# Kernel tuning notes

Measured on AMD Instinct MI355X. Metric: run time of the kernel, lower is better.

The kernel has to match this reference:

```python
import jax, jax.numpy as jnp
import numpy as np


def conv2d(x, w, b, pad):
    y = jax.lax.conv_general_dilated(x, w, (1, 1), [(pad, pad), (pad, pad)],
                                     dimension_numbers=('NCHW', 'OIHW', 'NCHW'))
    return y + b[None, :, None, None]


def setup_inputs() -> dict:
    key = jax.random.key(0)
    ks = jax.random.split(key, 24)
    bs, C, OC, K = 2, 64, 3, 3
    hi = wi = 96
    ho = wo = 192

    def _w(k, o, i, kh, kw):
        return jax.random.normal(k, (o, i, kh, kw), jnp.float32) / np.float32(np.sqrt(i * kh * kw))

    inp = {
        'x': jax.random.normal(ks[0], (bs, C, hi, wi), jnp.float32),
        'poseMap': jax.random.normal(ks[1], (1, 3, ho, wo), jnp.float32),
        'interMapY': jax.random.randint(ks[2], (ho, wo), 0, hi, jnp.int32),
        'interMapX': jax.random.randint(ks[3], (ho, wo), 0, wi, jnp.int32),
        # sigmaconv: 3x3 convs 64->64->64->2
        'sig_w1': _w(ks[4], 64, 64, 3, 3), 'sig_b1': jnp.zeros((64,), jnp.float32),
        'sig_w2': _w(ks[5], 64, 64, 3, 3), 'sig_b2': jnp.zeros((64,), jnp.float32),
        'sig_w3': _w(ks[6], 2, 64, 3, 3), 'sig_b3': jnp.zeros((2,), jnp.float32),
        # dwconv: 1x1 convs 3->64->256->C*K*K
        'dw_w1': _w(ks[7], 64, 3, 1, 1), 'dw_b1': jnp.zeros((64,), jnp.float32),
        'dw_w2': _w(ks[8], 256, 64, 1, 1), 'dw_b2': jnp.zeros((256,), jnp.float32),
        'dw_w3': _w(ks[9], C * K * K, 256, 1, 1), 'dw_b3': jnp.zeros((C * K * K,), jnp.float32),
        # pwconv: 1x1 convs 3->64->256->C*OC
        'pw_w1': _w(ks[10], 64, 3, 1, 1), 'pw_b1': jnp.zeros((64,), jnp.float32),
        'pw_w2': _w(ks[11], 256, 64, 1, 1), 'pw_b2': jnp.zeros((256,), jnp.float32),
        'pw_w3': _w(ks[12], C * OC, 256, 1, 1), 'pw_b3': jnp.zeros((C * OC,), jnp.float32),
    }
    return inp


def reference(x, poseMap, interMapY, interMapX,
              sig_w1, sig_b1, sig_w2, sig_b2, sig_w3, sig_b3,
              dw_w1, dw_b1, dw_w2, dw_b2, dw_w3, dw_b3,
              pw_w1, pw_b1, pw_w2, pw_b2, pw_w3, pw_b3):
    C, K, OC = 64, 3, 3
    bs, _, hi, wi = x.shape
    ho, wo = poseMap.shape[2], poseMap.shape[3]
    pad = K // 2

    p = jax.lax.stop_gradient(poseMap)  # original detaches poseMap
    # kernel-predict branches (1x1 conv MLPs over position map)
    dw = conv2d(jax.nn.relu(conv2d(jax.nn.relu(conv2d(p, dw_w1, dw_b1, 0)), dw_w2, dw_b2, 0)), dw_w3, dw_b3, 0)
    dw = dw.reshape(1, C, K * K, ho, wo)
    pw = conv2d(jax.nn.relu(conv2d(jax.nn.relu(conv2d(p, pw_w1, pw_b1, 0)), pw_w2, pw_b2, 0)), pw_w3, pw_b3, 0)
    pw = pw.reshape(C, OC, ho, wo)

    # unfold(x, K, padding=K//2): [bs, C, K*K, hi, wi], kernel taps row-major
    xp = jnp.pad(x, ((0, 0), (0, 0), (pad, pad), (pad, pad)))
    h = jnp.stack([xp[:, :, dy:dy + hi, dx:dx + wi]
                   for dy in range(K) for dx in range(K)], axis=2)
    # irregular spatial gather to HR grid: [bs, C, K*K, ho, wo]
    h = h[:, :, :, interMapY, interMapX]

    mean = jnp.sum(h * jax.nn.softmax(dw, axis=2), axis=2)  # [bs, C, ho, wo]
    sigma = conv2d(jax.nn.relu(conv2d(jax.nn.relu(conv2d(mean, sig_w1, sig_b1, 1)), sig_w2, sig_b2, 1)), sig_w3, sig_b3, 1)
    sigmad = sigma[:, 0:1, None, :, :]
    sigmar = sigma[:, 1:2, None, :, :]
    bw = sigmad * dw + sigmar * jnp.abs(h - mean[:, :, None, :, :])
    xa = jnp.sum(h * jax.nn.softmax(bw, axis=2), axis=2)  # [bs, C, ho, wo]
    out = jnp.einsum('bchw,cohw->bohw', xa, pw)  # [bs, OC, ho, wo]
    return out
```

## Files before the change

### kernel.cpp

```cpp
#include <hip/hip_runtime.h>
#include <hip/hip_bf16.h>

#define NPIX 36864

typedef __attribute__((ext_vector_type(8))) short short8;
typedef __attribute__((ext_vector_type(4))) short short4v;
typedef __attribute__((ext_vector_type(4))) float float4v;

__device__ inline unsigned short f2b(float x) {
    return __builtin_bit_cast(unsigned short, __float2bfloat16(x));
}
__device__ inline float b2f(unsigned short h) {
    return __uint_as_float(((unsigned int)h) << 16);
}

#define WB_TOTAL 312320
#define XCAST_N  1179648
__global__ __launch_bounds__(256) void prep_all(
    const float* __restrict__ dw2, const float* __restrict__ dw3,
    const float* __restrict__ pw2, const float* __restrict__ pw3,
    const float* __restrict__ sw1, const float* __restrict__ sw2,
    const float* __restrict__ sw3, unsigned short* __restrict__ wb,
    const float* __restrict__ x, unsigned short* __restrict__ xb)
{
    int i = blockIdx.x * 256 + threadIdx.x;
    if (i >= WB_TOTAL) {
        int j = i - WB_TOTAL;
        if (j < XCAST_N) xb[j] = f2b(x[j]);
        return;
    }
    unsigned short v;
    if (i < 16384)        v = f2b(dw2[i]);
    else if (i < 32768)   v = f2b(pw2[i - 16384]);
    else if (i < 180224)  v = f2b(dw3[i - 32768]);
    else if (i < 229376)  v = f2b(pw3[i - 180224]);
    else if (i < 266240) { int j = i - 229376; int t = j / 4096, r = j % 4096, oc = r / 64, ic = r % 64;
                           v = f2b(sw1[(oc * 64 + ic) * 9 + t]); }
    else if (i < 303104) { int j = i - 266240; int t = j / 4096, r = j % 4096, oc = r / 64, ic = r % 64;
                           v = f2b(sw2[(oc * 64 + ic) * 9 + t]); }
    else                 { int j = i - 303104; int t = j / 1024, r = j % 1024, oc = r / 64, ic = r % 64;
                           v = (oc < 2) ? f2b(sw3[(oc * 64 + ic) * 9 + t]) : (unsigned short)0; }
    wb[i] = v;
}

__global__ __launch_bounds__(512, 2) void mlp_fused(
    const float* __restrict__ pose,
    const float* __restrict__ w1A, const float* __restrict__ b1A,
    const float* __restrict__ w1B, const float* __restrict__ b1B,
    const unsigned short* __restrict__ w2A, const unsigned short* __restrict__ w2B,
    const float* __restrict__ b2A, const float* __restrict__ b2B,
    const unsigned short* __restrict__ w33,
    const float* __restrict__ b3A, const float* __restrict__ b3B,
    unsigned short* __restrict__ outA, unsigned short* __restrict__ outB)
{
    __shared__ unsigned short sh[69632];
    unsigned short* Ws  = sh;
    unsigned short* h2s = sh + 49152;
    unsigned short* h1s = sh + 65536;
    const int tid = threadIdx.x;
    const int u = blockIdx.y;
    const int chain = (u == 3) ? 1 : 0;
    const int w = tid >> 6, l = tid & 63;
    const int ln = l & 15, lkg = l >> 4, lk = lkg * 8;
    const float* w1 = chain ? w1B : w1A;
    const float* b1 = chain ? b1B : b1A;
    const unsigned short* w2 = chain ? w2B : w2A;
    const float* b2 = chain ? b2B : b2A;
    const int rowbase = chain ? 576 : u * 192;
    const int obase   = chain ? 0 : u * 192;
    const float* b3 = chain ? b3B : b3A;
    unsigned short* outp = chain ? outB : outA;

    for (int i = 0; i < 12; ++i) {
        const int chunk = (i * 8 + w) * 1024;
        int a  = chunk + l * 16;
        int ap = a ^ (((a >> 9) & 7) << 4);
        const unsigned short* gp =
            &w33[(size_t)(rowbase + (ap >> 9)) * 256 + ((ap & 511) >> 1)];
        __builtin_amdgcn_global_load_lds(
            (const __attribute__((address_space(1))) void*)gp,
            (__attribute__((address_space(3))) void*)((char*)Ws + chunk),
            16, 0, 0);
    }
    short8 Aw2[2][2];
    #pragma unroll
    for (int mt = 0; mt < 2; ++mt) {
        int ocr = w * 32 + mt * 16 + ln;
        Aw2[mt][0] = *(const short8*)&w2[(size_t)ocr * 64 + lk];
        Aw2[mt][1] = *(const short8*)&w2[(size_t)ocr * 64 + 32 + lk];
    }
    float w1r[8][3], b1r[8];
    #pragma unroll
    for (int j = 0; j < 8; ++j) {
        int oc = w * 8 + j;
        w1r[j][0] = w1[oc * 3]; w1r[j][1] = w1[oc * 3 + 1]; w1r[j][2] = w1[oc * 3 + 2];
        b1r[j] = b1[oc];
    }
    float b2r[2][4];
    #pragma unroll
    for (int mt = 0; mt < 2; ++mt) {
        int ocb = w * 32 + mt * 16 + lkg * 4;
        #pragma unroll
        for (int r = 0; r < 4; ++r) b2r[mt][r] = b2[ocb + r];
    }
    const int nh = w & 1, mb = w >> 1;
    float b3r[3][4];
    #pragma unroll
    for (int s = 0; s < 3; ++s) {
        int tr0 = (mb + s * 4) * 16 + lkg * 4;
        #pragma unroll
        for (int r = 0; r < 4; ++r) b3r[s][r] = b3[obase + tr0 + r];
    }
    const int pxbase = blockIdx.x * 576;
    float p0 = pose[pxbase + l], p1 = pose[NPIX + pxbase + l], p2 = pose[2 * NPIX + pxbase + l];

    for (int it = 0; it < 9; ++it) {
        const int px0 = pxbase + it * 64;
        {
            short8 s0;
            #pragma unroll
            for (int j = 0; j < 8; ++j) {
                float v = b1r[j] + w1r[j][0] * p0 + w1r[j][1] * p1 + w1r[j][2] * p2;
                s0[j] = (short)f2b(fmaxf(v, 0.f));
            }
            *(short8*)&h1s[w * 512 + l * 8] = s0;
        }
        float np0 = 0.f, np1 = 0.f, np2 = 0.f;
        if (it < 8) {
            int pxn = px0 + 64 + l;
            np0 = pose[pxn]; np1 = pose[NPIX + pxn]; np2 = pose[2 * NPIX + pxn];
        }
        __syncthreads();
        {
            short8 b0v[4], b1v[4];
            #pragma unroll
            for (int nt = 0; nt < 4; ++nt) {
                b0v[nt] = *(const short8*)&h1s[(lkg    ) * 512 + (nt * 16 + ln) * 8];
                b1v[nt] = *(const short8*)&h1s[(4 + lkg) * 512 + (nt * 16 + ln) * 8];
            }
            float4v acc2[2][4] = {};
            #pragma unroll
            for (int mt = 0; mt < 2; ++mt) {
                #pragma unroll
                for (int nt = 0; nt < 4; ++nt) {
                    acc2[mt][nt] = __builtin_amdgcn_mfma_f32_16x16x32_bf16(Aw2[mt][0], b0v[nt], acc2[mt][nt], 0, 0, 0);
                    acc2[mt][nt] = __builtin_amdgcn_mfma_f32_16x16x32_bf16(Aw2[mt][1], b1v[nt], acc2[mt][nt], 0, 0, 0);
                }
            }
            #pragma unroll
            for (int mt = 0; mt < 2; ++mt) {
                int ocb = w * 32 + mt * 16 + lkg * 4;
                int chk = ocb >> 3, pos = (lkg & 1) * 4;
                #pragma unroll
                for (int nt = 0; nt < 4; ++nt) {
                    int pxl = nt * 16 + ln;
                    short4v pk;
                    pk[0] = (short)f2b(fmaxf(acc2[mt][nt][0] + b2r[mt][0], 0.f));
                    pk[1] = (short)f2b(fmaxf(acc2[mt][nt][1] + b2r[mt][1], 0.f));
                    pk[2] = (short)f2b(fmaxf(acc2[mt][nt][2] + b2r[mt][2], 0.f));
                    pk[3] = (short)f2b(fmaxf(acc2[mt][nt][3] + b2r[mt][3], 0.f));
                    *(short4v*)&h2s[chk * 512 + pxl * 8 + pos] = pk;
                }
            }
        }
        __syncthreads();
        float4v acc[3][2] = {};
        {
            const int r0l = mb * 16 + ln;
            const int swz = (r0l & 7) << 4;
            const char* Wb = (const char*)Ws;
            #pragma unroll
            for (int kc = 0; kc < 8; ++kc) {
                short8 a0 = *(const short8*)(Wb + (((r0l      ) * 512 + kc * 64 + lk * 2) ^ swz));
                short8 a1 = *(const short8*)(Wb + (((r0l +  64) * 512 + kc * 64 + lk * 2) ^ swz));
                short8 a2 = *(const short8*)(Wb + (((r0l + 128) * 512 + kc * 64 + lk * 2) ^ swz));
                #pragma unroll
                for (int ni = 0; ni < 2; ++ni) {
                    int nt = nh * 2 + ni;
                    short8 b = *(const short8*)&h2s[(kc * 4 + lkg) * 512 + (nt * 16 + ln) * 8];
                    acc[0][ni] = __builtin_amdgcn_mfma_f32_16x16x32_bf16(a0, b, acc[0][ni], 0, 0, 0);
                    acc[1][ni] = __builtin_amdgcn_mfma_f32_16x16x32_bf16(a1, b, acc[1][ni], 0, 0, 0);
                    acc[2][ni] = __builtin_amdgcn_mfma_f32_16x16x32_bf16(a2, b, acc[2][ni], 0, 0, 0);
                }
            }
        }
        #pragma unroll
        for (int s = 0; s < 3; ++s) {
            const int tr0 = (mb + s * 4) * 16 + lkg * 4;
            #pragma unroll
            for (int r = 0; r < 4; ++r) {
                const size_t rowoff = (size_t)(obase + tr0 + r) * NPIX + px0;
                #pragma unroll
                for (int ni = 0; ni < 2; ++ni) {
                    int px = nh * 32 + ni * 16 + ln;
                    outp[rowoff + px] = f2b(acc[s][ni][r] + b3r[s][r]);
                }
            }
        }
        p0 = np0; p1 = np1; p2 = np2;
    }
}

__global__ __launch_bounds__(256, 2) void conv3x3_mfma4(
    const unsigned short* __restrict__ act, const unsigned short* __restrict__ wgt,
    const float* __restrict__ bias, unsigned short* __restrict__ out,
    int relu)
{
    constexpr int SP = 72;
    __shared__ unsigned short Bs[6 * 66 * SP];
    const int tid = threadIdx.x;
    int bx = blockIdx.x;
    const int xt = bx % 3; bx /= 3;
    const int yg = bx % 48; const int b = bx / 48;
    const int y0 = yg * 4;
    const int x0 = xt * 64;
    const size_t actb = (size_t)b * NPIX * 64;
    const int w = tid >> 6, l = tid & 63;
    const int ln = l & 15, lkg = l >> 4, lk = lkg * 8;
    const int mt = w;
    short8 Wr[9][2];
    #pragma unroll
    for (int t = 0; t < 9; ++t)
        #pragma unroll
        for (int hh = 0; hh < 2; ++hh)
            Wr[t][hh] = *(const short8*)&wgt[((size_t)t * 64 + mt * 16 + ln) * 64 + hh * 32 + lk];
    for (int s = tid; s < 396; s += 256) {
        int r = s / 66, i = s % 66;
        int yy = y0 + r - 1, xx = x0 + i - 1;
        unsigned short* dst = &Bs[(r * 66 + i) * SP];
        if (yy >= 0 && yy < 192 && xx >= 0 && xx < 192) {
            const unsigned short* src = &act[actb + (size_t)(yy * 192 + xx) * 64];
            #pragma unroll
            for (int j = 0; j < 8; ++j) *(short8*)(dst + j * 8) = *(const short8*)(src + j * 8);
        } else {
            short8 z = {};
            #pragma unroll
            for (int j = 0; j < 8; ++j) *(short8*)(dst + j * 8) = z;
        }
    }
    __syncthreads();
    float4v acc[4][4] = {};
    #pragma unroll
    for (int rp = 0; rp < 6; ++rp) {
        #pragma unroll
        for (int dx = 0; dx < 3; ++dx) {
            #pragma unroll
            for (int hh = 0; hh < 2; ++hh) {
                #pragma unroll
                for (int n = 0; n < 4; ++n) {
                    int slot = rp * 66 + n * 16 + ln + dx;
                    short8 bf = *(const short8*)&Bs[slot * SP + hh * 32 + lk];
                    #pragma unroll
                    for (int o = 0; o < 4; ++o) {
                        int r = rp - o;
                        if (r < 0 || r > 2) continue;
                        acc[o][n] = __builtin_amdgcn_mfma_f32_16x16x32_bf16(Wr[r * 3 + dx][hh], bf, acc[o][n], 0, 0, 0);
                    }
                }
            }
        }
    }
    #pragma unroll
    for (int o = 0; o < 4; ++o) {
        #pragma unroll
        for (int n = 0; n < 4; ++n) {
            int px = (y0 + o) * 192 + x0 + n * 16 + ln;
            int oc = mt * 16 + lkg * 4;
            float v0 = acc[o][n][0] + bias[oc + 0];
            float v1 = acc[o][n][1] + bias[oc + 1];
            float v2 = acc[o][n][2] + bias[oc + 2];
            float v3 = acc[o][n][3] + bias[oc + 3];
            if (relu) { v0 = fmaxf(v0, 0.f); v1 = fmaxf(v1, 0.f); v2 = fmaxf(v2, 0.f); v3 = fmaxf(v3, 0.f); }
            uint2 pk;
            pk.x = (unsigned int)f2b(v0) | (((unsigned int)f2b(v1)) << 16);
            pk.y = (unsigned int)f2b(v2) | (((unsigned int)f2b(v3)) << 16);
            *(uint2*)&out[((size_t)b * NPIX + px) * 64 + oc] = pk;
        }
    }
}

template<int MT>
__global__ __launch_bounds__(256) void conv3x3_mfma(
    const unsigned short* __restrict__ act, const unsigned short* __restrict__ wgt,
    const float* __restrict__ bias, unsigned short* __restrict__ out,
    int relu)
{
    constexpr int SP = 72;
    constexpr int OCP = MT * 16;
    __shared__ unsigned short Bs[4 * 66 * SP];
    const int tid = threadIdx.x;
    int bx = blockIdx.x;
    const int xt = bx % 3; bx /= 3;
    const int yg = bx % 96; const int b = bx / 96;
    const int y0 = yg * 2;
    const int x0 = xt * 64;
    const size_t actb = (size_t)b * NPIX * 64;
    const int w = tid >> 6, l = tid & 63;
    const int ln = l & 15, lkg = l >> 4, lk = lkg * 8;
    const int mt = (MT == 4) ? w : 0;
    short8 Wr[9][2];
    #pragma unroll
    for (int t = 0; t < 9; ++t)
        #pragma unroll
        for (int hh = 0; hh < 2; ++hh)
            Wr[t][hh] = *(const short8*)&wgt[((size_t)t * OCP + mt * 16 + ln) * 64 + hh * 32 + lk];
    for (int s = tid; s < 264; s += 256) {
        int r = s / 66, i = s % 66;
        int yy = y0 + r - 1, xx = x0 + i - 1;
        unsigned short* dst = &Bs[(r * 66 + i) * SP];
        if (yy >= 0 && yy < 192 && xx >= 0 && xx < 192) {
            const unsigned short* src = &act[actb + (size_t)(yy * 192 + xx) * 64];
            #pragma unroll
            for (int j = 0; j < 8; ++j) *(short8*)(dst + j * 8) = *(const short8*)(src + j * 8);
        } else {
            short8 z = {};
            #pragma unroll
            for (int j = 0; j < 8; ++j) *(short8*)(dst + j * 8) = z;
        }
    }
    __syncthreads();
    const int NT = (MT == 4) ? 4 : 1;
    const int ntb = (MT == 4) ? 0 : w;
    float4v acc[2][4] = {};
    #pragma unroll
    for (int t = 0; t < 9; ++t) {
        const int r = t / 3, dx = t % 3;
        #pragma unroll
        for (int hh = 0; hh < 2; ++hh) {
            #pragma unroll
            for (int o = 0; o < 2; ++o) {
                #pragma unroll
                for (int n = 0; n < 4; ++n) {
                    if (n >= NT) break;
                    int slot = (o + r) * 66 + (ntb + n) * 16 + ln + dx;
                    short8 bf = *(const short8*)&Bs[slot * SP + hh * 32 + lk];
                    acc[o][n] = __builtin_amdgcn_mfma_f32_16x16x32_bf16(Wr[t][hh], bf, acc[o][n], 0, 0, 0);
                }
            }
        }
    }
    #pragma unroll
    for (int o = 0; o < 2; ++o) {
        #pragma unroll
        for (int n = 0; n < 4; ++n) {
            if (n >= NT) break;
            int px = (y0 + o) * 192 + x0 + (ntb + n) * 16 + ln;
            if (MT == 4) {
                int oc = mt * 16 + lkg * 4;
                float v0 = acc[o][n][0] + bias[oc + 0];
                float v1 = acc[o][n][1] + bias[oc + 1];
                float v2 = acc[o][n][2] + bias[oc + 2];
                float v3 = acc[o][n][3] + bias[oc + 3];
                if (relu) { v0 = fmaxf(v0, 0.f); v1 = fmaxf(v1, 0.f); v2 = fmaxf(v2, 0.f); v3 = fmaxf(v3, 0.f); }
                uint2 pk;
                pk.x = (unsigned int)f2b(v0) | (((unsigned int)f2b(v1)) << 16);
                pk.y = (unsigned int)f2b(v2) | (((unsigned int)f2b(v3)) << 16);
                *(uint2*)&out[((size_t)b * NPIX + px) * 64 + oc] = pk;
            } else if (lkg == 0) {
                float v0 = acc[o][n][0] + bias[0];
                float v1 = acc[o][n][1] + bias[1];
                out[((size_t)b * 2 + 0) * NPIX + px] = f2b(v0);
                out[((size_t)b * 2 + 1) * NPIX + px] = f2b(v1);
            }
        }
    }
}

#define PLSZ 10192
__global__ __launch_bounds__(256) void mean_k(
    const unsigned short* __restrict__ xb, const int* __restrict__ imy, const int* __restrict__ imx,
    const unsigned short* __restrict__ dw, unsigned short* __restrict__ mean_cm)
{
    __shared__ unsigned short pl[PLSZ];
    const int c = blockIdx.y;
    const int px0 = blockIdx.x * 1024;
    const int tid = threadIdx.x;
    {
        short8 z = {};
        short8* pf = (short8*)pl;
        for (int i = tid; i < PLSZ / 8; i += 256) pf[i] = z;
    }
    float wk[4][9];
    int base[4];
    #pragma unroll
    for (int q = 0; q < 4; ++q) {
        int px = px0 + q * 256 + tid;
        base[q] = imy[px] * 104 + imx[px] + 3;
        float d[9];
        #pragma unroll
        for (int k = 0; k < 9; ++k) d[k] = b2f(dw[(size_t)(c * 9 + k) * NPIX + px]);
        float m = d[0];
        #pragma unroll
        for (int k = 1; k < 9; ++k) m = fmaxf(m, d[k]);
        float s = 0.f;
        #pragma unroll
        for (int k = 0; k < 9; ++k) { wk[q][k] = __expf(d[k] - m); s += wk[q][k]; }
        float inv = 1.f / s;
        #pragma unroll
        for (int k = 0; k < 9; ++k) wk[q][k] *= inv;
    }
    #pragma unroll
    for (int b = 0; b < 2; ++b) {
        __syncthreads();
        const unsigned short* xp = xb + (size_t)(b * 64 + c) * 9216;
        for (int i = tid; i < 96 * 12; i += 256) {
            int row = i / 12, ch = i % 12;
            const short4v* src = (const short4v*)&xp[row * 96 + ch * 8];
            unsigned short* dd = &pl[(row + 1) * 104 + 4 + ch * 8];
            *(short4v*)dd = src[0];
            *(short4v*)(dd + 4) = src[1];
        }
        __syncthreads();
        #pragma unroll
        for (int q = 0; q < 4; ++q) {
            int px = px0 + q * 256 + tid;
            float a = 0.f;
            #pragma unroll
            for (int k = 0; k < 9; ++k)
                a += wk[q][k] * b2f(pl[base[q] + (k / 3) * 104 + (k % 3)]);
            mean_cm[(size_t)(b * 64 + c) * NPIX + px] = f2b(a);
        }
    }
}

__global__ __launch_bounds__(256) void tr_k(
    const unsigned short* __restrict__ in, unsigned short* __restrict__ out)
{
    __shared__ unsigned short T[64 * 68];
    int px0 = blockIdx.x * 64;
    int b = blockIdx.y;
    int tid = threadIdx.x;
    for (int i = tid; i < 4096; i += 256) {
        int c = i >> 6, p = i & 63;
        T[p * 68 + c] = in[(size_t)(b * 64 + c) * NPIX + px0 + p];
    }
    __syncthreads();
    for (int i = tid; i < 4096; i += 256) {
        int p = i >> 6, c = i & 63;
        out[((size_t)b * NPIX + px0 + p) * 64 + c] = T[p * 68 + c];
    }
}

__global__ __launch_bounds__(256) void xa_k(
    const unsigned short* __restrict__ xb, const int* __restrict__ imy, const int* __restrict__ imx,
    const unsigned short* __restrict__ dw, const unsigned short* __restrict__ mean_cm,
    const unsigned short* __restrict__ sigma, unsigned short* __restrict__ xab)
{
    __shared__ unsigned short pl[PLSZ];
    const int c = blockIdx.y;
    const int px0 = blockIdx.x * 1024;
    const int tid = threadIdx.x;
    {
        short8 z = {};
        short8* pf = (short8*)pl;
        for (int i = tid; i < PLSZ / 8; i += 256) pf[i] = z;
    }
    float d[4][9];
    int base[4];
    #pragma unroll
    for (int q = 0; q < 4; ++q) {
        int px = px0 + q * 256 + tid;
        base[q] = imy[px] * 104 + imx[px] + 3;
        #pragma unroll
        for (int k = 0; k < 9; ++k) d[q][k] = b2f(dw[(size_t)(c * 9 + k) * NPIX + px]);
    }
    #pragma unroll
    for (int b = 0; b < 2; ++b) {
        __syncthreads();
        const unsigned short* xp = xb + (size_t)(b * 64 + c) * 9216;
        for (int i = tid; i < 96 * 12; i += 256) {
            int row = i / 12, ch = i % 12;
            const short4v* src = (const short4v*)&xp[row * 96 + ch * 8];
            unsigned short* dd = &pl[(row + 1) * 104 + 4 + ch * 8];
            *(short4v*)dd = src[0];
            *(short4v*)(dd + 4) = src[1];
        }
        __syncthreads();
        #pragma unroll
        for (int q = 0; q < 4; ++q) {
            int px = px0 + q * 256 + tid;
            float mn = b2f(mean_cm[(size_t)(b * 64 + c) * NPIX + px]);
            float sd = b2f(sigma[((size_t)b * 2 + 0) * NPIX + px]);
            float sr = b2f(sigma[((size_t)b * 2 + 1) * NPIX + px]);
            float h[9], bw[9];
            #pragma unroll
            for (int k = 0; k < 9; ++k) {
                h[k] = b2f(pl[base[q] + (k / 3) * 104 + (k % 3)]);
                bw[k] = sd * d[q][k] + sr * fabsf(h[k] - mn);
            }
            float m = bw[0];
            #pragma unroll
            for (int k = 1; k < 9; ++k) m = fmaxf(m, bw[k]);
            float s = 0.f, a = 0.f;
            #pragma unroll
            for (int k = 0; k < 9; ++k) { float e = __expf(bw[k] - m); s += e; a += e * h[k]; }
            xab[(size_t)(b * 64 + c) * NPIX + px] = f2b(a / s);
        }
    }
}

__global__ __launch_bounds__(256) void einsum_k(
    const unsigned short* __restrict__ xab, const unsigned short* __restrict__ pw,
    float* __restrict__ out)
{
    __shared__ float red[3][4][64];
    const int tid = threadIdx.x;
    const int pxl = tid & 63, cq = tid >> 6;
    const int px = blockIdx.x * 64 + pxl;
    const int b = blockIdx.y;
    float a0 = 0.f, a1 = 0.f, a2 = 0.f;
    #pragma unroll
    for (int ci = 0; ci < 16; ++ci) {
        int c = cq * 16 + ci;
        float v = b2f(xab[(size_t)(b * 64 + c) * NPIX + px]);
        a0 += v * b2f(pw[(size_t)(c * 3 + 0) * NPIX + px]);
        a1 += v * b2f(pw[(size_t)(c * 3 + 1) * NPIX + px]);
        a2 += v * b2f(pw[(size_t)(c * 3 + 2) * NPIX + px]);
    }
    red[0][cq][pxl] = a0;
    red[1][cq][pxl] = a1;
    red[2][cq][pxl] = a2;
    __syncthreads();
    if (cq < 3) {
        float s = red[cq][0][pxl] + red[cq][1][pxl] + red[cq][2][pxl] + red[cq][3][pxl];
        out[((size_t)b * 3 + cq) * NPIX + px] = s;
    }
}

extern "C" void kernel_launch(void* const* d_in, const int* in_sizes, int n_in,
                              void* d_out, int out_size, void* d_ws, size_t ws_size,
                              hipStream_t stream)
{
    (void)in_sizes; (void)n_in; (void)out_size; (void)ws_size;
    const float* x      = (const float*)d_in[0];
    const float* pose   = (const float*)d_in[1];
    const int*   imy    = (const int*)d_in[2];
    const int*   imx    = (const int*)d_in[3];
    const float* sig_w1 = (const float*)d_in[4];
    const float* sig_b1 = (const float*)d_in[5];
    const float* sig_w2 = (const float*)d_in[6];
    const float* sig_b2 = (const float*)d_in[7];
    const float* sig_w3 = (const float*)d_in[8];
    const float* sig_b3 = (const float*)d_in[9];
    const float* dw_w1  = (const float*)d_in[10];
    const float* dw_b1  = (const float*)d_in[11];
    const float* dw_w2  = (const float*)d_in[12];
    const float* dw_b2  = (const float*)d_in[13];
    const float* dw_w3  = (const float*)d_in[14];
    const float* dw_b3  = (const float*)d_in[15];
    const float* pw_w1  = (const float*)d_in[16];
    const float* pw_b1  = (const float*)d_in[17];
    const float* pw_w2  = (const float*)d_in[18];
    const float* pw_b2  = (const float*)d_in[19];
    const float* pw_w3  = (const float*)d_in[20];
    const float* pw_b3  = (const float*)d_in[21];
    float* out = (float*)d_out;

    unsigned short* ws = (unsigned short*)d_ws;
    size_t off = 0;
    unsigned short* wb      = ws + off; off += WB_TOTAL;
    unsigned short* xb16    = ws + off; off += (size_t)XCAST_N;
    unsigned short* dwbuf   = ws + off; off += (size_t)576 * NPIX;
    unsigned short* pwbuf   = ws + off; off += (size_t)192 * NPIX;
    unsigned short* mean_cm = ws + off; off += (size_t)2 * 64 * NPIX;
    unsigned short* mean_pm = ws + off; off += (size_t)2 * NPIX * 64;
    unsigned short* s1      = ws + off; off += (size_t)2 * NPIX * 64;
    unsigned short* s2      = ws + off; off += (size_t)2 * NPIX * 64;
    unsigned short* sigma   = ws + off; off += (size_t)2 * 2 * NPIX;
    unsigned short* xab     = ws + off; off += (size_t)2 * 64 * NPIX;

    unsigned short* w_dw2 = wb + 0;
    unsigned short* w_pw2 = wb + 16384;
    unsigned short* w_33  = wb + 32768;
    unsigned short* w_s1t = wb + 229376;
    unsigned short* w_s2t = wb + 266240;
    unsigned short* w_s3t = wb + 303104;

    dim3 blk(256);
    prep_all<<<dim3((WB_TOTAL + XCAST_N + 255) / 256), blk, 0, stream>>>(
        dw_w2, dw_w3, pw_w2, pw_w3, sig_w1, sig_w2, sig_w3, wb, x, xb16);
    mlp_fused<<<dim3(64, 4), dim3(512), 0, stream>>>(
        pose, dw_w1, dw_b1, pw_w1, pw_b1, w_dw2, w_pw2, dw_b2, pw_b2,
        w_33, dw_b3, pw_b3, dwbuf, pwbuf);
    mean_k<<<dim3(36, 64), blk, 0, stream>>>(xb16, imy, imx, dwbuf, mean_cm);
    tr_k<<<dim3(576, 2), blk, 0, stream>>>(mean_cm, mean_pm);
    conv3x3_mfma4<<<dim3(288), blk, 0, stream>>>(mean_pm, w_s1t, sig_b1, s1, 1);
    conv3x3_mfma4<<<dim3(288), blk, 0, stream>>>(s1,      w_s2t, sig_b2, s2, 1);
    conv3x3_mfma<1><<<dim3(576), blk, 0, stream>>>(s2,     w_s3t, sig_b3, sigma, 0);
    xa_k<<<dim3(36, 64), blk, 0, stream>>>(xb16, imy, imx, dwbuf, mean_cm, sigma, xab);
    einsum_k<<<dim3(576, 2), blk, 0, stream>>>(xab, pwbuf, out);
}
```

Before: 228.6 us.

## Remove prep kernel by converting weights and input to bf16 inside consumers

The separate prep_all launch that cast weights and x to bf16 into workspace is removed. Each consumer kernel (mlp_fused, conv3x3, mean_k, xa_k) now reads the fp32 tensors directly and converts them in registers before staging to LDS or loading MFMA operands. This saves one launch and a round-trip write and read of the bf16 copies. In exchange, fp32 reads double the bytes per element, conversion work is repeated across blocks, the conv weight loads become strided scalar gathers, and the async global_load_lds path for w3 is replaced by synchronous loads.

```diff
diff --git a/kernel.cpp b/kernel.cpp
--- a/kernel.cpp
+++ b/kernel.cpp
@@ -12,44 +12,15 @@
 }
 __device__ inline float b2f(unsigned short h) {
     return __uint_as_float(((unsigned int)h) << 16);
-}
-
-#define WB_TOTAL 312320
-#define XCAST_N  1179648
-__global__ __launch_bounds__(256) void prep_all(
-    const float* __restrict__ dw2, const float* __restrict__ dw3,
-    const float* __restrict__ pw2, const float* __restrict__ pw3,
-    const float* __restrict__ sw1, const float* __restrict__ sw2,
-    const float* __restrict__ sw3, unsigned short* __restrict__ wb,
-    const float* __restrict__ x, unsigned short* __restrict__ xb)
-{
-    int i = blockIdx.x * 256 + threadIdx.x;
-    if (i >= WB_TOTAL) {
-        int j = i - WB_TOTAL;
-        if (j < XCAST_N) xb[j] = f2b(x[j]);
-        return;
-    }
-    unsigned short v;
-    if (i < 16384)        v = f2b(dw2[i]);
-    else if (i < 32768)   v = f2b(pw2[i - 16384]);
-    else if (i < 180224)  v = f2b(dw3[i - 32768]);
-    else if (i < 229376)  v = f2b(pw3[i - 180224]);
-    else if (i < 266240) { int j = i - 229376; int t = j / 4096, r = j % 4096, oc = r / 64, ic = r % 64;
-                           v = f2b(sw1[(oc * 64 + ic) * 9 + t]); }
-    else if (i < 303104) { int j = i - 266240; int t = j / 4096, r = j % 4096, oc = r / 64, ic = r % 64;
-                           v = f2b(sw2[(oc * 64 + ic) * 9 + t]); }
-    else                 { int j = i - 303104; int t = j / 1024, r = j % 1024, oc = r / 64, ic = r % 64;
-                           v = (oc < 2) ? f2b(sw3[(oc * 64 + ic) * 9 + t]) : (unsigned short)0; }
-    wb[i] = v;
 }
 
 __global__ __launch_bounds__(512, 2) void mlp_fused(
     const float* __restrict__ pose,
     const float* __restrict__ w1A, const float* __restrict__ b1A,
     const float* __restrict__ w1B, const float* __restrict__ b1B,
-    const unsigned short* __restrict__ w2A, const unsigned short* __restrict__ w2B,
+    const float* __restrict__ w2Af, const float* __restrict__ w2Bf,
     const float* __restrict__ b2A, const float* __restrict__ b2B,
-    const unsigned short* __restrict__ w33,
+    const float* __restrict__ w3Af, const float* __restrict__ w3Bf,
     const float* __restrict__ b3A, const float* __restrict__ b3B,
     unsigned short* __restrict__ outA, unsigned short* __restrict__ outB)
 {
@@ -64,10 +35,11 @@
     const int ln = l & 15, lkg = l >> 4, lk = lkg * 8;
     const float* w1 = chain ? w1B : w1A;
     const float* b1 = chain ? b1B : b1A;
-    const unsigned short* w2 = chain ? w2B : w2A;
+    const float* w2f = chain ? w2Bf : w2Af;
     const float* b2 = chain ? b2B : b2A;
-    const int rowbase = chain ? 576 : u * 192;
-    const int obase   = chain ? 0 : u * 192;
+    const float* w3f = chain ? w3Bf : w3Af;
+    const int rb    = chain ? 0 : u * 192;
+    const int obase = chain ? 0 : u * 192;
     const float* b3 = chain ? b3B : b3A;
     unsigned short* outp = chain ? outB : outA;
 
@@ -75,19 +47,32 @@
         const int chunk = (i * 8 + w) * 1024;
         int a  = chunk + l * 16;
         int ap = a ^ (((a >> 9) & 7) << 4);
-        const unsigned short* gp =
-            &w33[(size_t)(rowbase + (ap >> 9)) * 256 + ((ap & 511) >> 1)];
-        __builtin_amdgcn_global_load_lds(
-            (const __attribute__((address_space(1))) void*)gp,
-            (__attribute__((address_space(3))) void*)((char*)Ws + chunk),
-            16, 0, 0);
+        const float* gp = &w3f[(size_t)(rb + (ap >> 9)) * 256 + ((ap & 511) >> 1)];
+        float4v f0 = *(const float4v*)gp;
+        float4v f1 = *(const float4v*)(gp + 4);
+        short8 s;
+        s[0] = (short)f2b(f0[0]); s[1] = (short)f2b(f0[1]);
+        s[2] = (short)f2b(f0[2]); s[3] = (short)f2b(f0[3]);
+        s[4] = (short)f2b(f1[0]); s[5] = (short)f2b(f1[1]);
+        s[6] = (short)f2b(f1[2]); s[7] = (short)f2b(f1[3]);
+        *(short8*)((char*)Ws + a) = s;
     }
     short8 Aw2[2][2];
     #pragma unroll
     for (int mt = 0; mt < 2; ++mt) {
         int ocr = w * 32 + mt * 16 + ln;
-        Aw2[mt][0] = *(const short8*)&w2[(size_t)ocr * 64 + lk];
-        Aw2[mt][1] = *(const short8*)&w2[(size_t)ocr * 64 + 32 + lk];
+        #pragma unroll
+        for (int hh = 0; hh < 2; ++hh) {
+            const float* gp = &w2f[(size_t)ocr * 64 + hh * 32 + lk];
+            float4v f0 = *(const float4v*)gp;
+            float4v f1 = *(const float4v*)(gp + 4);
+            short8 s;
+            s[0] = (short)f2b(f0[0]); s[1] = (short)f2b(f0[1]);
+            s[2] = (short)f2b(f0[2]); s[3] = (short)f2b(f0[3]);
+            s[4] = (short)f2b(f1[0]); s[5] = (short)f2b(f1[1]);
+            s[6] = (short)f2b(f1[2]); s[7] = (short)f2b(f1[3]);
+            Aw2[mt][hh] = s;
+        }
     }
     float w1r[8][3], b1r[8];
     #pragma unroll
@@ -202,7 +187,7 @@
 }
 
 __global__ __launch_bounds__(256, 2) void conv3x3_mfma4(
-    const unsigned short* __restrict__ act, const unsigned short* __restrict__ wgt,
+    const unsigned short* __restrict__ act, const float* __restrict__ wgt,
     const float* __restrict__ bias, unsigned short* __restrict__ out,
     int relu)
 {
@@ -222,8 +207,13 @@
     #pragma unroll
     for (int t = 0; t < 9; ++t)
         #pragma unroll
-        for (int hh = 0; hh < 2; ++hh)
-            Wr[t][hh] = *(const short8*)&wgt[((size_t)t * 64 + mt * 16 + ln) * 64 + hh * 32 + lk];
+        for (int hh = 0; hh < 2; ++hh) {
+            short8 s;
+            #pragma unroll
+            for (int j = 0; j < 8; ++j)
+                s[j] = (short)f2b(wgt[((size_t)(mt * 16 + ln) * 64 + hh * 32 + lk + j) * 9 + t]);
+            Wr[t][hh] = s;
+        }
     for (int s = tid; s < 396; s += 256) {
         int r = s / 66, i = s % 66;
         int yy = y0 + r - 1, xx = x0 + i - 1;
@@ -279,14 +269,11 @@
     }
 }
 
-template<int MT>
-__global__ __launch_bounds__(256) void conv3x3_mfma(
-    const unsigned short* __restrict__ act, const unsigned short* __restrict__ wgt,
-    const float* __restrict__ bias, unsigned short* __restrict__ out,
-    int relu)
+__global__ __launch_bounds__(256) void conv3x3_sig(
+    const unsigned short* __restrict__ act, const float* __restrict__ wgt,
+    const float* __restrict__ bias, unsigned short* __restrict__ out)
 {
     constexpr int SP = 72;
-    constexpr int OCP = MT * 16;
     __shared__ unsigned short Bs[4 * 66 * SP];
     const int tid = threadIdx.x;
     int bx = blockIdx.x;
@@ -297,13 +284,17 @@
     const size_t actb = (size_t)b * NPIX * 64;
     const int w = tid >> 6, l = tid & 63;
     const int ln = l & 15, lkg = l >> 4, lk = lkg * 8;
-    const int mt = (MT == 4) ? w : 0;
     short8 Wr[9][2];
     #pragma unroll
     for (int t = 0; t < 9; ++t)
         #pragma unroll
-        for (int hh = 0; hh < 2; ++hh)
-            Wr[t][hh] = *(const short8*)&wgt[((size_t)t * OCP + mt * 16 + ln) * 64 + hh * 32 + lk];
+        for (int hh = 0; hh < 2; ++hh) {
+            short8 s;
+            #pragma unroll
+            for (int j = 0; j < 8; ++j)
+                s[j] = (ln < 2) ? (short)f2b(wgt[((size_t)ln * 64 + hh * 32 + lk + j) * 9 + t]) : (short)0;
+            Wr[t][hh] = s;
+        }
     for (int s = tid; s < 264; s += 256) {
         int r = s / 66, i = s % 66;
         int yy = y0 + r - 1, xx = x0 + i - 1;
@@ -319,9 +310,7 @@
         }
     }
     __syncthreads();
-    const int NT = (MT == 4) ? 4 : 1;
-    const int ntb = (MT == 4) ? 0 : w;
-    float4v acc[2][4] = {};
+    float4v acc[2] = {};
     #pragma unroll
     for (int t = 0; t < 9; ++t) {
         const int r = t / 3, dx = t % 3;
@@ -329,46 +318,25 @@
         for (int hh = 0; hh < 2; ++hh) {
             #pragma unroll
             for (int o = 0; o < 2; ++o) {
-                #pragma unroll
-                for (int n = 0; n < 4; ++n) {
-                    if (n >= NT) break;
-                    int slot = (o + r) * 66 + (ntb + n) * 16 + ln + dx;
-                    short8 bf = *(const short8*)&Bs[slot * SP + hh * 32 + lk];
-                    acc[o][n] = __builtin_amdgcn_mfma_f32_16x16x32_bf16(Wr[t][hh], bf, acc[o][n], 0, 0, 0);
-                }
+                int slot = (o + r) * 66 + w * 16 + ln + dx;
+                short8 bf = *(const short8*)&Bs[slot * SP + hh * 32 + lk];
+                acc[o] = __builtin_amdgcn_mfma_f32_16x16x32_bf16(Wr[t][hh], bf, acc[o], 0, 0, 0);
             }
         }
     }
     #pragma unroll
     for (int o = 0; o < 2; ++o) {
-        #pragma unroll
-        for (int n = 0; n < 4; ++n) {
-            if (n >= NT) break;
-            int px = (y0 + o) * 192 + x0 + (ntb + n) * 16 + ln;
-            if (MT == 4) {
-                int oc = mt * 16 + lkg * 4;
-                float v0 = acc[o][n][0] + bias[oc + 0];
-                float v1 = acc[o][n][1] + bias[oc + 1];
-                float v2 = acc[o][n][2] + bias[oc + 2];
-                float v3 = acc[o][n][3] + bias[oc + 3];
-                if (relu) { v0 = fmaxf(v0, 0.f); v1 = fmaxf(v1, 0.f); v2 = fmaxf(v2, 0.f); v3 = fmaxf(v3, 0.f); }
-                uint2 pk;
-                pk.x = (unsigned int)f2b(v0) | (((unsigned int)f2b(v1)) << 16);
-                pk.y = (unsigned int)f2b(v2) | (((unsigned int)f2b(v3)) << 16);
-                *(uint2*)&out[((size_t)b * NPIX + px) * 64 + oc] = pk;
-            } else if (lkg == 0) {
-                float v0 = acc[o][n][0] + bias[0];
-                float v1 = acc[o][n][1] + bias[1];
-                out[((size_t)b * 2 + 0) * NPIX + px] = f2b(v0);
-                out[((size_t)b * 2 + 1) * NPIX + px] = f2b(v1);
-            }
+        if (lkg == 0) {
+            int px = (y0 + o) * 192 + x0 + w * 16 + ln;
+            out[((size_t)b * 2 + 0) * NPIX + px] = f2b(acc[o][0] + bias[0]);
+            out[((size_t)b * 2 + 1) * NPIX + px] = f2b(acc[o][1] + bias[1]);
         }
     }
 }
 
 #define PLSZ 10192
 __global__ __launch_bounds__(256) void mean_k(
-    const unsigned short* __restrict__ xb, const int* __restrict__ imy, const int* __restrict__ imx,
+    const float* __restrict__ x, const int* __restrict__ imy, const int* __restrict__ imx,
     const unsigned short* __restrict__ dw, unsigned short* __restrict__ mean_cm)
 {
     __shared__ unsigned short pl[PLSZ];
@@ -402,13 +370,19 @@
     #pragma unroll
     for (int b = 0; b < 2; ++b) {
         __syncthreads();
-        const unsigned short* xp = xb + (size_t)(b * 64 + c) * 9216;
+        const float* xp = x + (size_t)(b * 64 + c) * 9216;
         for (int i = tid; i < 96 * 12; i += 256) {
             int row = i / 12, ch = i % 12;
-            const short4v* src = (const short4v*)&xp[row * 96 + ch * 8];
+            const float4v* src = (const float4v*)&xp[row * 96 + ch * 8];
+            float4v f0 = src[0], f1 = src[1];
+            short4v lo, hi;
+            lo[0] = (short)f2b(f0[0]); lo[1] = (short)f2b(f0[1]);
+            lo[2] = (short)f2b(f0[2]); lo[3] = (short)f2b(f0[3]);
+            hi[0] = (short)f2b(f1[0]); hi[1] = (short)f2b(f1[1]);
+            hi[2] = (short)f2b(f1[2]); hi[3] = (short)f2b(f1[3]);
             unsigned short* dd = &pl[(row + 1) * 104 + 4 + ch * 8];
-            *(short4v*)dd = src[0];
-            *(short4v*)(dd + 4) = src[1];
+            *(short4v*)dd = lo;
+            *(short4v*)(dd + 4) = hi;
         }
         __syncthreads();
         #pragma unroll
@@ -442,7 +416,7 @@
 }
 
 __global__ __launch_bounds__(256) void xa_k(
-    const unsigned short* __restrict__ xb, const int* __restrict__ imy, const int* __restrict__ imx,
+    const float* __restrict__ x, const int* __restrict__ imy, const int* __restrict__ imx,
     const unsigned short* __restrict__ dw, const unsigned short* __restrict__ mean_cm,
     const unsigned short* __restrict__ sigma, unsigned short* __restrict__ xab)
 {
@@ -467,13 +441,19 @@
     #pragma unroll
     for (int b = 0; b < 2; ++b) {
         __syncthreads();
-        const unsigned short* xp = xb + (size_t)(b * 64 + c) * 9216;
+        const float* xp = x + (size_t)(b * 64 + c) * 9216;
         for (int i = tid; i < 96 * 12; i += 256) {
             int row = i / 12, ch = i % 12;
-            const short4v* src = (const short4v*)&xp[row * 96 + ch * 8];
+            const float4v* src = (const float4v*)&xp[row * 96 + ch * 8];
+            float4v f0 = src[0], f1 = src[1];
+            short4v lo, hi;
+            lo[0] = (short)f2b(f0[0]); lo[1] = (short)f2b(f0[1]);
+            lo[2] = (short)f2b(f0[2]); lo[3] = (short)f2b(f0[3]);
+            hi[0] = (short)f2b(f1[0]); hi[1] = (short)f2b(f1[1]);
+            hi[2] = (short)f2b(f1[2]); hi[3] = (short)f2b(f1[3]);
             unsigned short* dd = &pl[(row + 1) * 104 + 4 + ch * 8];
-            *(short4v*)dd = src[0];
-            *(short4v*)(dd + 4) = src[1];
+            *(short4v*)dd = lo;
+            *(short4v*)(dd + 4) = hi;
         }
         __syncthreads();
         #pragma unroll
@@ -558,8 +538,6 @@
 
     unsigned short* ws = (unsigned short*)d_ws;
     size_t off = 0;
-    unsigned short* wb      = ws + off; off += WB_TOTAL;
-    unsigned short* xb16    = ws + off; off += (size_t)XCAST_N;
     unsigned short* dwbuf   = ws + off; off += (size_t)576 * NPIX;
     unsigned short* pwbuf   = ws + off; off += (size_t)192 * NPIX;
     unsigned short* mean_cm = ws + off; off += (size_t)2 * 64 * NPIX;
@@ -569,24 +547,15 @@
     unsigned short* sigma   = ws + off; off += (size_t)2 * 2 * NPIX;
     unsigned short* xab     = ws + off; off += (size_t)2 * 64 * NPIX;
 
-    unsigned short* w_dw2 = wb + 0;
-    unsigned short* w_pw2 = wb + 16384;
-    unsigned short* w_33  = wb + 32768;
-    unsigned short* w_s1t = wb + 229376;
-    unsigned short* w_s2t = wb + 266240;
-    unsigned short* w_s3t = wb + 303104;
-
     dim3 blk(256);
-    prep_all<<<dim3((WB_TOTAL + XCAST_N + 255) / 256), blk, 0, stream>>>(
-        dw_w2, dw_w3, pw_w2, pw_w3, sig_w1, sig_w2, sig_w3, wb, x, xb16);
     mlp_fused<<<dim3(64, 4), dim3(512), 0, stream>>>(
-        pose, dw_w1, dw_b1, pw_w1, pw_b1, w_dw2, w_pw2, dw_b2, pw_b2,
-        w_33, dw_b3, pw_b3, dwbuf, pwbuf);
-    mean_k<<<dim3(36, 64), blk, 0, stream>>>(xb16, imy, imx, dwbuf, mean_cm);
+        pose, dw_w1, dw_b1, pw_w1, pw_b1, dw_w2, pw_w2, dw_b2, pw_b2,
+        dw_w3, pw_w3, dw_b3, pw_b3, dwbuf, pwbuf);
+    mean_k<<<dim3(36, 64), blk, 0, stream>>>(x, imy, imx, dwbuf, mean_cm);
     tr_k<<<dim3(576, 2), blk, 0, stream>>>(mean_cm, mean_pm);
-    conv3x3_mfma4<<<dim3(288), blk, 0, stream>>>(mean_pm, w_s1t, sig_b1, s1, 1);
-    conv3x3_mfma4<<<dim3(288), blk, 0, stream>>>(s1,      w_s2t, sig_b2, s2, 1);
-    conv3x3_mfma<1><<<dim3(576), blk, 0, stream>>>(s2,     w_s3t, sig_b3, sigma, 0);
-    xa_k<<<dim3(36, 64), blk, 0, stream>>>(xb16, imy, imx, dwbuf, mean_cm, sigma, xab);
+    conv3x3_mfma4<<<dim3(288), blk, 0, stream>>>(mean_pm, sig_w1, sig_b1, s1, 1);
+    conv3x3_mfma4<<<dim3(288), blk, 0, stream>>>(s1,      sig_w2, sig_b2, s2, 1);
+    conv3x3_sig<<<dim3(576), blk, 0, stream>>>(s2, sig_w3, sig_b3, sigma);
+    xa_k<<<dim3(36, 64), blk, 0, stream>>>(x, imy, imx, dwbuf, mean_cm, sigma, xab);
     einsum_k<<<dim3(576, 2), blk, 0, stream>>>(xab, pwbuf, out);
 }
```

Result: slower. 258.4 us (+13.1%).
